# Kernel optimization log

Hardware: AMD Instinct MI355X
Metric: run time of the kernel (lower is better)

The kernel has to match this reference:

```python
import jax, jax.numpy as jnp
import numpy as np

B, C, G, N_OBJ = 256, 1019, 7, 16
IMG_SIZE = 448.0

def setup_inputs() -> dict:
    key = jax.random.key(0)
    k1, k2, k3, k4 = jax.random.split(key, 4)
    outputs = jax.random.normal(k1, (B, 5 + C, G, G), dtype=jnp.float32)
    boxes = jax.random.uniform(k2, (B, N_OBJ, 4), dtype=jnp.float32, minval=0.0, maxval=IMG_SIZE)
    labels = jax.random.randint(k3, (B, N_OBJ), 1, C + 1, dtype=jnp.int32)  # 1..C (code uses label-1)
    coords = jax.random.randint(k4, (B, N_OBJ, 2), 0, G, dtype=jnp.int32)   # (x, y) grid cells
    # objectness target matrix: 1.0 at cells containing an object, else 0 (soft CE target)
    bidx = jnp.arange(B)[:, None]
    obj = jnp.zeros((B, G, G), jnp.float32).at[bidx, coords[..., 1], coords[..., 0]].set(1.0)
    obj_matrix = obj.reshape(B, G * G)
    return {"outputs": outputs, "boxes": boxes, "labels": labels, "coords": coords, "obj_matrix": obj_matrix}

def reference(outputs, boxes, labels, coords, obj_matrix):
    Bn = outputs.shape[0]
    # objectness CE with soft targets: mean over batch of -sum(target * log_softmax(pred))
    p_obj = outputs[:, 0].reshape(Bn, -1)                      # [B, 49]
    cel_obj = jnp.mean(-jnp.sum(obj_matrix * jax.nn.log_softmax(p_obj, axis=-1), axis=-1))
    # gather per-object predictions at grid cells (x=coords[...,0], y=coords[...,1])
    bidx = jnp.arange(Bn)[:, None]
    y = coords[..., 1]
    x = coords[..., 0]
    pred_boxes = outputs[:, 1:5][bidx, :, y, x]                # [B, N_OBJ, 4]
    tgt_scaled = jnp.round(boxes / IMG_SIZE * 10.0) / 10.0     # np.round(x/IMG_SIZE, 1)
    bb_loss = jnp.sum((tgt_scaled - pred_boxes) ** 2) / Bn
    # per-object class cross-entropy, summed then divided by batch
    pred_labels = outputs[:, 5:][bidx, :, y, x]                # [B, N_OBJ, C]
    logp = jax.nn.log_softmax(pred_labels, axis=-1)
    ce = -jnp.take_along_axis(logp, (labels - 1)[..., None].astype(jnp.int32), axis=-1)
    cel_class = jnp.sum(ce) / Bn
    return cel_obj + bb_loss + cel_class
```

## Files before the change

kernel.cpp:

```cpp
#include <hip/hip_runtime.h>

#define BATCH 256
#define NCLS  1019
#define GRID  7
#define NOBJ  16
#define PLANE 49
#define NCH   1024
#define SLAB  (NCH * PLANE)
#define TPB   1024
#define NWAVE 16

__global__ __launch_bounds__(TPB) void yolo_loss_kernel(
    const float* __restrict__ outputs,
    const float* __restrict__ boxes,
    const int*   __restrict__ labels,
    const int*   __restrict__ coords,
    const float* __restrict__ obj_matrix,
    float* __restrict__ out)
{
    const int b    = blockIdx.x;
    const int t    = threadIdx.x;
    const int lane = t & 63;
    const int w    = t >> 6;

    __shared__ float s_part[NWAVE][64];
    __shared__ float s_sumexp[64];
    __shared__ int   s_pos[NOBJ];
    __shared__ int   s_cl[NOBJ];
    __shared__ float s_red;

    const float* ob = outputs + (size_t)b * SLAB;

    if (t == 0) s_red = 0.0f;
    if (t < NOBJ) {
        int x = coords[(b * NOBJ + t) * 2 + 0];
        int y = coords[(b * NOBJ + t) * 2 + 1];
        s_pos[t] = y * GRID + x;
        s_cl[t]  = labels[b * NOBJ + t] - 1;
    }
    __syncthreads();

    if (w == 1) {
        float l = (lane < PLANE) ? ob[lane] : 0.0f;
        float s = (lane < PLANE) ? __expf(l) : 0.0f;
#pragma unroll
        for (int off = 32; off > 0; off >>= 1)
            s += __shfl_xor(s, off, 64);
        float lse = __logf(s);
        float m = (lane < PLANE) ? obj_matrix[b * PLANE + lane] : 0.0f;
        float contrib = (lane < PLANE) ? -m * (l - lse) : 0.0f;
#pragma unroll
        for (int off = 32; off > 0; off >>= 1)
            contrib += __shfl_xor(contrib, off, 64);
        if (lane == 0) atomicAdd(&s_red, contrib);
    }

    if (w == 2) {
        int o = lane >> 2, k = lane & 3;
        float pred = ob[(size_t)(1 + k) * PLANE + s_pos[o]];
        float tb   = boxes[(b * NOBJ + o) * 4 + k];
        float tgt  = rintf(tb * (10.0f / 448.0f)) * 0.1f;
        float d    = tgt - pred;
        float sq   = d * d;
#pragma unroll
        for (int off = 32; off > 0; off >>= 1)
            sq += __shfl_xor(sq, off, 64);
        if (lane == 0) atomicAdd(&s_red, sq);
    }

    const int   p = (lane < PLANE) ? lane : 0;
    const float m = (lane < PLANE) ? 1.0f : 0.0f;
    float a0 = 0.0f, a1 = 0.0f, a2 = 0.0f, a3 = 0.0f;

    int c = 5 + w;
    for (; c + 48 < NCH; c += 64) {
        float v0 = ob[(c     ) * PLANE + p];
        float v1 = ob[(c + 16) * PLANE + p];
        float v2 = ob[(c + 32) * PLANE + p];
        float v3 = ob[(c + 48) * PLANE + p];
        a0 += m * __expf(v0);
        a1 += m * __expf(v1);
        a2 += m * __expf(v2);
        a3 += m * __expf(v3);
    }
    for (; c < NCH; c += 16)
        a0 += m * __expf(ob[c * PLANE + p]);

    s_part[w][lane] = (a0 + a1) + (a2 + a3);
    __syncthreads();

    if (w == 0) {
        float s = 0.0f;
#pragma unroll
        for (int i = 0; i < NWAVE; ++i) s += s_part[i][lane];
        s_sumexp[lane] = s;
    }
    __syncthreads();

    if (w == 0 && lane < NOBJ) {
        float se = s_sumexp[s_pos[lane]];
        float tl = ob[(size_t)(5 + s_cl[lane]) * PLANE + s_pos[lane]];
        float ce = __logf(se) - tl;
        atomicAdd(&s_red, ce);
    }
    __syncthreads();

    if (t == 0) atomicAdd(out, s_red * (1.0f / (float)BATCH));
}

extern "C" void kernel_launch(void* const* d_in, const int* in_sizes, int n_in,
                              void* d_out, int out_size, void* d_ws, size_t ws_size,
                              hipStream_t stream) {
    const float* outputs    = (const float*)d_in[0];
    const float* boxes      = (const float*)d_in[1];
    const int*   labels     = (const int*)d_in[2];
    const int*   coords     = (const int*)d_in[3];
    const float* obj_matrix = (const float*)d_in[4];
    float* out = (float*)d_out;

    hipMemsetAsync(out, 0, sizeof(float), stream);
    yolo_loss_kernel<<<BATCH, TPB, 0, stream>>>(outputs, boxes, labels, coords,
                                                obj_matrix, out);
}
```

Baseline: 99.38 us.

## Load the channel slab as float4 groups and remap per-cell sums through shared memory

```diff
diff --git a/kernel.cpp b/kernel.cpp
--- a/kernel.cpp
+++ b/kernel.cpp
@@ -9,6 +9,7 @@
 #define SLAB  (NCH * PLANE)
 #define TPB   1024
 #define NWAVE 16
+#define NGRP  256
 
 __global__ __launch_bounds__(TPB) void yolo_loss_kernel(
     const float* __restrict__ outputs,
@@ -23,13 +24,14 @@
     const int lane = t & 63;
     const int w    = t >> 6;
 
-    __shared__ float s_part[NWAVE][64];
-    __shared__ float s_sumexp[64];
+    __shared__ float s_slot[NWAVE][4 * PLANE];
+    __shared__ float s_sum[PLANE];
     __shared__ int   s_pos[NOBJ];
     __shared__ int   s_cl[NOBJ];
     __shared__ float s_red;
 
-    const float* ob = outputs + (size_t)b * SLAB;
+    const float*  ob  = outputs + (size_t)b * SLAB;
+    const float4* ob4 = (const float4*)ob;
 
     if (t == 0) s_red = 0.0f;
     if (t < NOBJ) {
@@ -47,8 +49,8 @@
         for (int off = 32; off > 0; off >>= 1)
             s += __shfl_xor(s, off, 64);
         float lse = __logf(s);
-        float m = (lane < PLANE) ? obj_matrix[b * PLANE + lane] : 0.0f;
-        float contrib = (lane < PLANE) ? -m * (l - lse) : 0.0f;
+        float mm = (lane < PLANE) ? obj_matrix[b * PLANE + lane] : 0.0f;
+        float contrib = (lane < PLANE) ? -mm * (l - lse) : 0.0f;
 #pragma unroll
         for (int off = 32; off > 0; off >>= 1)
             contrib += __shfl_xor(contrib, off, 64);
@@ -68,37 +70,50 @@
         if (lane == 0) atomicAdd(&s_red, sq);
     }
 
-    const int   p = (lane < PLANE) ? lane : 0;
-    const float m = (lane < PLANE) ? 1.0f : 0.0f;
+    const bool  act = lane < PLANE;
+    const float m   = act ? 1.0f : 0.0f;
+    const int   lc  = act ? lane : 0;
     float a0 = 0.0f, a1 = 0.0f, a2 = 0.0f, a3 = 0.0f;
 
-    int c = 5 + w;
-    for (; c + 48 < NCH; c += 64) {
-        float v0 = ob[(c     ) * PLANE + p];
-        float v1 = ob[(c + 16) * PLANE + p];
-        float v2 = ob[(c + 32) * PLANE + p];
-        float v3 = ob[(c + 48) * PLANE + p];
-        a0 += m * __expf(v0);
-        a1 += m * __expf(v1);
-        a2 += m * __expf(v2);
-        a3 += m * __expf(v3);
+    const float4* base = ob4 + (size_t)PLANE * w + lc;
+    for (int i = 0; i < 16; i += 4) {
+        float4 v0 = base[(size_t)PLANE * NWAVE * (i + 0)];
+        float4 v1 = base[(size_t)PLANE * NWAVE * (i + 1)];
+        float4 v2 = base[(size_t)PLANE * NWAVE * (i + 2)];
+        float4 v3 = base[(size_t)PLANE * NWAVE * (i + 3)];
+        a0 += m * __expf(v0.x); a1 += m * __expf(v0.y);
+        a2 += m * __expf(v0.z); a3 += m * __expf(v0.w);
+        a0 += m * __expf(v1.x); a1 += m * __expf(v1.y);
+        a2 += m * __expf(v1.z); a3 += m * __expf(v1.w);
+        a0 += m * __expf(v2.x); a1 += m * __expf(v2.y);
+        a2 += m * __expf(v2.z); a3 += m * __expf(v2.w);
+        a0 += m * __expf(v3.x); a1 += m * __expf(v3.y);
+        a2 += m * __expf(v3.z); a3 += m * __expf(v3.w);
     }
-    for (; c < NCH; c += 16)
-        a0 += m * __expf(ob[c * PLANE + p]);
-
-    s_part[w][lane] = (a0 + a1) + (a2 + a3);
+    if (act) {
+        float4* dst = (float4*)&s_slot[w][4 * lc];
+        *dst = make_float4(a0, a1, a2, a3);
+    }
     __syncthreads();
 
-    if (w == 0) {
+    if (w == 0 && lane < PLANE) {
         float s = 0.0f;
 #pragma unroll
-        for (int i = 0; i < NWAVE; ++i) s += s_part[i][lane];
-        s_sumexp[lane] = s;
+        for (int ww = 0; ww < NWAVE; ++ww) {
+#pragma unroll
+            for (int k = 0; k < 4; ++k)
+                s += s_slot[ww][lane + PLANE * k];
+        }
+        float corr = 0.0f;
+#pragma unroll
+        for (int r = 0; r < 5; ++r)
+            corr += __expf(ob[r * PLANE + lane]);
+        s_sum[lane] = s - corr;
     }
     __syncthreads();
 
     if (w == 0 && lane < NOBJ) {
-        float se = s_sumexp[s_pos[lane]];
+        float se = s_sum[s_pos[lane]];
         float tl = ob[(size_t)(5 + s_cl[lane]) * PLANE + s_pos[lane]];
         float ce = __logf(se) - tl;
         atomicAdd(&s_red, ce);
```

Result: faster. 93.20 us (-6.2%).
